# Optimization experiments

Measured on AMD Instinct MI355X. Metric: run time of the kernel, lower is better.

## Reference

```python
import jax, jax.numpy as jnp
import numpy as np

N_NODES = 20000
N_EDGES = 100000
MUL = 128          # channels per irrep
R = 8              # radial (edge scalar) features
H = 64             # radial MLP hidden width
SILU_NORM = 1.6790390826      # e3nn normalize2mom constant for SiLU
INV_SQRT3 = 1.0 / np.sqrt(3.0)   # wigner-3j values for l<=1 paths
PW_0E = np.sqrt(0.5)   # e3nn path weight: out dim 1, fan-in 2 paths
PW_1O = np.sqrt(1.5)   # e3nn path weight: out dim 3, fan-in 2 paths


def setup_inputs() -> dict:
    key = jax.random.key(0)
    ks = jax.random.split(key, 12)
    return dict(
        node_feats=jax.random.normal(ks[0], (N_NODES, 4 * MUL), jnp.float32),
        edge_attrs=jax.random.normal(ks[1], (N_EDGES, 4), jnp.float32),   # SH: 1x0e+1x1o
        edge_feats=jax.random.normal(ks[2], (N_EDGES, R), jnp.float32),
        edge_index=jax.random.randint(ks[3], (2, N_EDGES), 0, N_NODES),
        W_up_s=jax.random.normal(ks[4], (MUL, MUL), jnp.float32),
        W_up_v=jax.random.normal(ks[5], (MUL, MUL), jnp.float32),
        mlp_w0=jax.random.normal(ks[6], (R, H), jnp.float32),
        mlp_w1=jax.random.normal(ks[7], (H, H), jnp.float32),
        mlp_w2=jax.random.normal(ks[8], (H, H), jnp.float32),
        mlp_w3=jax.random.normal(ks[9], (H, 4 * MUL), jnp.float32),
        W_out_s=jax.random.normal(ks[10], (2 * MUL, MUL), jnp.float32),
        W_out_v=jax.random.normal(ks[11], (2 * MUL, MUL), jnp.float32),
    )


def reference(node_feats, edge_attrs, edge_feats, edge_index,
              W_up_s, W_up_v, mlp_w0, mlp_w1, mlp_w2, mlp_w3,
              W_out_s, W_out_v):
    sender = edge_index[0]
    # split node feats into irrep blocks: 128x0e then 128x1o (channel-major [u, m])
    s = node_feats[:, :MUL]                       # [N, 128]
    v = node_feats[:, MUL:].reshape(-1, MUL, 3)   # [N, 128, 3]
    # linear_up: per-irrep e3nn Linear, fan_in-normalized
    s = (s @ W_up_s) / np.sqrt(MUL)
    v = jnp.einsum('nui,uw->nwi', v, W_up_v) / np.sqrt(MUL)
    # radial MLP -> per-edge tensor-product weights (e3nn FullyConnectedNet)
    act = lambda x: jax.nn.silu(x) * SILU_NORM
    h = act(edge_feats @ (mlp_w0 / np.sqrt(R)))
    h = act(h @ (mlp_w1 / np.sqrt(H)))
    h = act(h @ (mlp_w2 / np.sqrt(H)))
    tpw = h @ (mlp_w3 / np.sqrt(H))               # [E, 4*128]
    w00, w01, w10, w11 = jnp.split(tpw, 4, axis=1)  # instruction order of weight_numel
    # gather sender node features per edge
    ss = s[sender]                                # [E, 128]
    vs = v[sender]                                # [E, 128, 3]
    sh0 = edge_attrs[:, :1]                       # [E, 1]  scalar SH
    sh1 = edge_attrs[:, 1:]                       # [E, 3]  l=1 SH
    # uvu CG tensor product paths (l<=1 wigner-3j)
    a0 = PW_0E * w00 * ss * sh0                                   # 0e x 0e -> 0e
    a1 = (PW_1O * INV_SQRT3) * (w01 * ss)[:, :, None] * sh1[:, None, :]   # 0e x 1o -> 1o
    b1 = (PW_1O * INV_SQRT3) * (w10 * sh0)[:, :, None] * vs              # 1o x 0e -> 1o
    b0 = (PW_0E * INV_SQRT3) * w11 * jnp.einsum('eui,ei->eu', vs, sh1)   # 1o x 1o -> 0e
    # irreps_mid sorted+simplified: 256x0e + 256x1o
    mid_s = jnp.concatenate([a0, b0], axis=1)     # [E, 256]
    mid_v = jnp.concatenate([a1, b1], axis=1)     # [E, 256, 3]
    # final per-irrep linear to target 128x0e + 128x1o
    out_s = (mid_s @ W_out_s) / np.sqrt(2 * MUL)
    out_v = jnp.einsum('eui,uw->ewi', mid_v, W_out_v) / np.sqrt(2 * MUL)
    return jnp.concatenate([out_s, out_v.reshape(out_v.shape[0], 3 * MUL)], axis=1)
```

## Files before the change

kernel.cpp:

```cpp
#include <hip/hip_runtime.h>
#include <stdint.h>

#define N_NODES 20000
#define N_EDGES 100000

typedef __bf16 bf16;
typedef bf16  bf16x8 __attribute__((ext_vector_type(8)));
typedef float f32x4  __attribute__((ext_vector_type(4)));

__device__ __forceinline__ f32x4 mfma16(bf16x8 a, bf16x8 b, f32x4 c) {
  return __builtin_amdgcn_mfma_f32_16x16x32_bf16(a, b, c, 0, 0, 0);
}

__device__ __forceinline__ float silu_(float y) {
  return y / (1.0f + __expf(-y));
}

#define OFF_W0T   0u
#define OFF_W1T   4096u
#define OFF_W2T   12288u
#define OFF_W3T   20480u
#define OFF_WOS   86016u
#define OFF_WOV   151552u
#define OFF_WST   217088u
#define OFF_WVT   249856u
#define OFF_SUP   282624u
#define OFF_VUP   5402624u

__global__ __launch_bounds__(256) void k0_prep(
    const float* __restrict__ wus, const float* __restrict__ wuv,
    const float* __restrict__ w0,  const float* __restrict__ w1,
    const float* __restrict__ w2,  const float* __restrict__ w3,
    const float* __restrict__ wos_g, const float* __restrict__ wov_g,
    char* __restrict__ ws) {
  const int idx = blockIdx.x * 256 + threadIdx.x;
  bf16* W0T = (bf16*)(ws + OFF_W0T);
  bf16* W1T = (bf16*)(ws + OFF_W1T);
  bf16* W2T = (bf16*)(ws + OFF_W2T);
  bf16* W3T = (bf16*)(ws + OFF_W3T);
  bf16* WOS = (bf16*)(ws + OFF_WOS);
  bf16* WOV = (bf16*)(ws + OFF_WOV);
  bf16* WST = (bf16*)(ws + OFF_WST);
  bf16* WVT = (bf16*)(ws + OFF_WVT);

  const float cS   = 0.08838834764831845f;
  const float c0   = 0.35355339059327373f;
  const float c12  = 1.6790390826f / 8.0f;
  const float cosA = 0.04419417382415922f;
  const float cosB = 0.025515518153991442f;
  const float cov  = 0.04419417382415922f;

  if (idx < 16384) {
    int w = idx >> 7, u = idx & 127;
    WST[idx] = (bf16)(wus[u * 128 + w] * cS);
    WVT[idx] = (bf16)(wuv[u * 128 + w] * cS);
  }
  if (idx < 2048) {
    int h = idx >> 5, r = idx & 31;
    W0T[idx] = (bf16)((r < 8) ? w0[r * 64 + h] * c0 : 0.0f);
  }
  if (idx < 4096) {
    int h = idx >> 6, k = idx & 63;
    W1T[idx] = (bf16)(w1[k * 64 + h] * c12);
    W2T[idx] = (bf16)(w2[k * 64 + h] * c12);
  }
  {
    int j = idx >> 6, k = idx & 63;
    W3T[idx] = (bf16)(w3[k * 512 + j] * c12);
    int w = idx >> 8, u = idx & 255;
    WOS[idx] = (bf16)(wos_g[u * 128 + w] * ((u < 128) ? cosA : cosB));
    WOV[idx] = (bf16)(wov_g[u * 128 + w] * cov);
  }
}

__global__ __launch_bounds__(256, 4) void k1_nodeup(const float* __restrict__ nf,
                                                    char* __restrict__ ws) {
  __shared__ __align__(16) bf16 tiles[4][32 * 136];
  const int n0 = blockIdx.x * 32;
  const int t = threadIdx.x;

  #pragma unroll
  for (int p = 0; p < 16; p++) {
    int idx = p * 256 + t;
    int r = idx >> 7, c4 = idx & 127;
    const float4 f = *(const float4*)&nf[(size_t)(n0 + r) * 512 + c4 * 4];
    float vals[4] = {f.x, f.y, f.z, f.w};
    #pragma unroll
    for (int e2 = 0; e2 < 4; e2++) {
      int g = c4 * 4 + e2;
      if (g < 128) {
        tiles[0][r * 136 + g] = (bf16)vals[e2];
      } else {
        int gg = g - 128;
        int u = gg / 3, i = gg - 3 * u;
        tiles[1 + i][r * 136 + u] = (bf16)vals[e2];
      }
    }
  }
  __syncthreads();

  const int wv = t >> 6, lane = t & 63;
  const int m = lane & 15, q = lane >> 4;
  const bf16* BT = (const bf16*)(ws + ((wv == 0) ? OFF_WST : OFF_WVT));
  const bf16* At = tiles[wv];

  const f32x4 z = {0.f, 0.f, 0.f, 0.f};
  f32x4 acc[2][8] = {{z, z, z, z, z, z, z, z}, {z, z, z, z, z, z, z, z}};
  #pragma unroll
  for (int kk = 0; kk < 128; kk += 32) {
    bf16x8 af0 = *(const bf16x8*)&At[m * 136 + kk + q * 8];
    bf16x8 af1 = *(const bf16x8*)&At[(16 + m) * 136 + kk + q * 8];
    #pragma unroll
    for (int nt = 0; nt < 8; nt++) {
      bf16x8 bfr = *(const bf16x8*)&BT[(nt * 16 + m) * 128 + kk + q * 8];
      acc[0][nt] = mfma16(af0, bfr, acc[0][nt]);
      acc[1][nt] = mfma16(af1, bfr, acc[1][nt]);
    }
  }

  bf16* sup = (bf16*)(ws + OFF_SUP);
  bf16* vup = (bf16*)(ws + OFF_VUP);
  #pragma unroll
  for (int rt = 0; rt < 2; rt++) {
    #pragma unroll
    for (int nt = 0; nt < 8; nt++) {
      int col = nt * 16 + m;
      #pragma unroll
      for (int r = 0; r < 4; r++) {
        int node = n0 + rt * 16 + q * 4 + r;
        if (wv == 0) sup[node * 128 + col] = (bf16)acc[rt][nt][r];
        else         vup[node * 384 + (wv - 1) * 128 + col] = (bf16)acc[rt][nt][r];
      }
    }
  }
}

#define SM_TPW 0
#define SM_A   33280
#define SM_A0  33280
#define SM_H0  (33280 + 2560)
#define SM_H1  (33280 + 7168)
#define SM_SND 51712
#define SM_ATT 51840
#define TPW_LD 520

__global__ __launch_bounds__(256, 3) void k23_fused(
    const float* __restrict__ efeat, const float* __restrict__ attrs,
    const int* __restrict__ sender, const char* __restrict__ ws,
    float* __restrict__ out) {
  __shared__ __align__(16) char smem[52352];
  bf16* tpwL = (bf16*)(smem + SM_TPW);
  bf16* A    = (bf16*)(smem + SM_A);
  bf16* A0e  = (bf16*)(smem + SM_A0);
  bf16* h0   = (bf16*)(smem + SM_H0);
  bf16* h1   = (bf16*)(smem + SM_H1);
  int*  sLDS = (int*)(smem + SM_SND);
  float* aLDS = (float*)(smem + SM_ATT);

  const int e0 = blockIdx.x * 32;
  const int t = threadIdx.x;
  const int wv = t >> 6, lane = t & 63;
  const int m = lane & 15, q = lane >> 4;
  const f32x4 z = {0.f, 0.f, 0.f, 0.f};

  {
    int r = t >> 3, k = t & 7;
    A0e[r * 40 + k] = (bf16)efeat[(e0 + r) * 8 + k];
    #pragma unroll
    for (int pp = 0; pp < 3; pp++) {
      int pidx = t * 3 + pp;
      int r2 = pidx / 24, k2 = 8 + pidx % 24;
      A0e[r2 * 40 + k2] = (bf16)0.0f;
    }
    if (t < 32) sLDS[t] = sender[e0 + t];
    if (t < 128) aLDS[t] = attrs[e0 * 4 + t];
  }
  __syncthreads();

  const bf16* W0T = (const bf16*)(ws + OFF_W0T);
  const bf16* W1T = (const bf16*)(ws + OFF_W1T);
  const bf16* W2T = (const bf16*)(ws + OFF_W2T);
  const bf16* W3T = (const bf16*)(ws + OFF_W3T);

  const int rt = wv & 1, nh = wv >> 1;

  {
    f32x4 acc[2] = {z, z};
    bf16x8 af = *(const bf16x8*)&A0e[(rt * 16 + m) * 40 + q * 8];
    #pragma unroll
    for (int ntl = 0; ntl < 2; ntl++) {
      int ntg = nh * 2 + ntl;
      bf16x8 bfr = *(const bf16x8*)&W0T[(ntg * 16 + m) * 32 + q * 8];
      acc[ntl] = mfma16(af, bfr, acc[ntl]);
    }
    __syncthreads();
    #pragma unroll
    for (int ntl = 0; ntl < 2; ntl++)
      #pragma unroll
      for (int r = 0; r < 4; r++)
        h0[(rt * 16 + q * 4 + r) * 72 + (nh * 2 + ntl) * 16 + m] = (bf16)silu_(acc[ntl][r]);
  }
  __syncthreads();

  {
    f32x4 acc[2] = {z, z};
    #pragma unroll
    for (int kk = 0; kk < 64; kk += 32) {
      bf16x8 af = *(const bf16x8*)&h0[(rt * 16 + m) * 72 + kk + q * 8];
      #pragma unroll
      for (int ntl = 0; ntl < 2; ntl++) {
        int ntg = nh * 2 + ntl;
        bf16x8 bfr = *(const bf16x8*)&W1T[(ntg * 16 + m) * 64 + kk + q * 8];
        acc[ntl] = mfma16(af, bfr, acc[ntl]);
      }
    }
    __syncthreads();
    #pragma unroll
    for (int ntl = 0; ntl < 2; ntl++)
      #pragma unroll
      for (int r = 0; r < 4; r++)
        h1[(rt * 16 + q * 4 + r) * 72 + (nh * 2 + ntl) * 16 + m] = (bf16)silu_(acc[ntl][r]);
  }
  __syncthreads();

  {
    f32x4 acc[2] = {z, z};
    #pragma unroll
    for (int kk = 0; kk < 64; kk += 32) {
      bf16x8 af = *(const bf16x8*)&h1[(rt * 16 + m) * 72 + kk + q * 8];
      #pragma unroll
      for (int ntl = 0; ntl < 2; ntl++) {
        int ntg = nh * 2 + ntl;
        bf16x8 bfr = *(const bf16x8*)&W2T[(ntg * 16 + m) * 64 + kk + q * 8];
        acc[ntl] = mfma16(af, bfr, acc[ntl]);
      }
    }
    __syncthreads();
    #pragma unroll
    for (int ntl = 0; ntl < 2; ntl++)
      #pragma unroll
      for (int r = 0; r < 4; r++)
        h0[(rt * 16 + q * 4 + r) * 72 + (nh * 2 + ntl) * 16 + m] = (bf16)silu_(acc[ntl][r]);
  }
  __syncthreads();

  {
    bf16x8 af0 = *(const bf16x8*)&h0[(rt * 16 + m) * 72 + 0  + q * 8];
    bf16x8 af1 = *(const bf16x8*)&h0[(rt * 16 + m) * 72 + 32 + q * 8];
    #pragma unroll 4
    for (int i = 0; i < 16; i++) {
      int ntg = nh * 16 + i;
      f32x4 acc = z;
      bf16x8 b0 = *(const bf16x8*)&W3T[(ntg * 16 + m) * 64 + q * 8];
      bf16x8 b1 = *(const bf16x8*)&W3T[(ntg * 16 + m) * 64 + 32 + q * 8];
      acc = mfma16(af0, b0, acc);
      acc = mfma16(af1, b1, acc);
      int col = ntg * 16 + m;
      #pragma unroll
      for (int r = 0; r < 4; r++)
        tpwL[(rt * 16 + q * 4 + r) * TPW_LD + col] = (bf16)acc[r];
    }
  }
  __syncthreads();

  const bf16* sup = (const bf16*)(ws + OFF_SUP);
  const bf16* vup = (const bf16*)(ws + OFF_VUP);
  const bf16* WB = (const bf16*)(ws + ((wv == 0) ? OFF_WOS : OFF_WOV));

  const int srow = t >> 1;
  const int kh = (t & 1) * 32;
  const bool isS = (srow < 32);
  const int ii = isS ? 0 : ((srow - 32) >> 5);
  const int eL = isS ? srow : ((srow - 32) & 31);
  const int se = sLDS[eL];
  const float s0  = aLDS[eL * 4 + 0];
  const float s1x = aLDS[eL * 4 + 1];
  const float s1y = aLDS[eL * 4 + 2];
  const float s1z = aLDS[eL * 4 + 3];
  const float s1i = (ii == 0) ? s1x : ((ii == 1) ? s1y : s1z);
  const bf16* tpr = tpwL + eL * TPW_LD;
  const bf16* supR = sup + se * 128;
  const bf16* vupR = vup + se * 384;

  f32x4 acc0[8] = {z, z, z, z, z, z, z, z};
  f32x4 acc1[8] = {z, z, z, z, z, z, z, z};

  for (int kc = 0; kc < 4; kc++) {
    if (kc) __syncthreads();
    if (kc < 2) {
      const int ub = kc * 64 + kh;
      if (isS) {
        #pragma unroll
        for (int j0 = 0; j0 < 32; j0 += 8) {
          bf16x8 tv = *(const bf16x8*)&tpr[ub + j0];
          bf16x8 sv = *(const bf16x8*)&supR[ub + j0];
          bf16x8 o;
          #pragma unroll
          for (int e = 0; e < 8; e++)
            o[e] = (bf16)((float)tv[e] * (float)sv[e] * s0);
          *(bf16x8*)&A[srow * 72 + kh + j0] = o;
        }
      } else {
        #pragma unroll
        for (int j0 = 0; j0 < 32; j0 += 8) {
          bf16x8 tv = *(const bf16x8*)&tpr[128 + ub + j0];
          bf16x8 sv = *(const bf16x8*)&supR[ub + j0];
          bf16x8 o;
          #pragma unroll
          for (int e = 0; e < 8; e++)
            o[e] = (bf16)((float)tv[e] * (float)sv[e] * s1i);
          *(bf16x8*)&A[srow * 72 + kh + j0] = o;
        }
      }
    } else {
      const int ub = (kc - 2) * 64 + kh;
      if (isS) {
        #pragma unroll
        for (int j0 = 0; j0 < 32; j0 += 8) {
          bf16x8 tv = *(const bf16x8*)&tpr[384 + ub + j0];
          bf16x8 vx = *(const bf16x8*)&vupR[ub + j0];
          bf16x8 vy = *(const bf16x8*)&vupR[128 + ub + j0];
          bf16x8 vz = *(const bf16x8*)&vupR[256 + ub + j0];
          bf16x8 o;
          #pragma unroll
          for (int e = 0; e < 8; e++) {
            float dv = (float)vx[e] * s1x + (float)vy[e] * s1y + (float)vz[e] * s1z;
            o[e] = (bf16)((float)tv[e] * dv);
          }
          *(bf16x8*)&A[srow * 72 + kh + j0] = o;
        }
      } else {
        #pragma unroll
        for (int j0 = 0; j0 < 32; j0 += 8) {
          bf16x8 tv = *(const bf16x8*)&tpr[256 + ub + j0];
          bf16x8 vv = *(const bf16x8*)&vupR[ii * 128 + ub + j0];
          bf16x8 o;
          #pragma unroll
          for (int e = 0; e < 8; e++)
            o[e] = (bf16)((float)tv[e] * s0 * (float)vv[e]);
          *(bf16x8*)&A[srow * 72 + kh + j0] = o;
        }
      }
    }
    __syncthreads();

    const int kb = kc * 64;
    #pragma unroll
    for (int kk = 0; kk < 64; kk += 32) {
      bf16x8 af0 = *(const bf16x8*)&A[(wv * 32 + m) * 72 + kk + q * 8];
      bf16x8 af1 = *(const bf16x8*)&A[(wv * 32 + 16 + m) * 72 + kk + q * 8];
      #pragma unroll
      for (int nt = 0; nt < 8; nt++) {
        bf16x8 bfr = *(const bf16x8*)&WB[(nt * 16 + m) * 256 + kb + kk + q * 8];
        acc0[nt] = mfma16(af0, bfr, acc0[nt]);
        acc1[nt] = mfma16(af1, bfr, acc1[nt]);
      }
    }
  }

  #pragma unroll
  for (int b = 0; b < 2; b++) {
    const f32x4* accp = b ? acc1 : acc0;
    int rb = wv * 32 + b * 16 + q * 4;
    #pragma unroll
    for (int nt = 0; nt < 8; nt++) {
      int col = nt * 16 + m;
      #pragma unroll
      for (int r = 0; r < 4; r++) {
        int row = rb + r;
        float v = accp[nt][r];
        if (wv == 0) {
          out[(size_t)(e0 + row) * 512 + col] = v;
        } else {
          int i2 = (row - 32) >> 5, eL2 = (row - 32) & 31;
          out[(size_t)(e0 + eL2) * 512 + 128 + 3 * col + i2] = v;
        }
      }
    }
  }
}

extern "C" void kernel_launch(void* const* d_in, const int* in_sizes, int n_in,
                              void* d_out, int out_size, void* d_ws, size_t ws_size,
                              hipStream_t stream) {
  const float* node_feats = (const float*)d_in[0];
  const float* edge_attrs = (const float*)d_in[1];
  const float* edge_feats = (const float*)d_in[2];
  const int*   edge_index = (const int*)d_in[3];
  const float* W_up_s = (const float*)d_in[4];
  const float* W_up_v = (const float*)d_in[5];
  const float* w0 = (const float*)d_in[6];
  const float* w1 = (const float*)d_in[7];
  const float* w2 = (const float*)d_in[8];
  const float* w3 = (const float*)d_in[9];
  const float* Wos = (const float*)d_in[10];
  const float* Wov = (const float*)d_in[11];
  float* out = (float*)d_out;
  char* ws = (char*)d_ws;

  k0_prep<<<dim3(128), dim3(256), 0, stream>>>(W_up_s, W_up_v, w0, w1, w2, w3,
                                               Wos, Wov, ws);
  k1_nodeup<<<dim3(625), dim3(256), 0, stream>>>(node_feats, ws);
  k23_fused<<<dim3(3125), dim3(256), 0, stream>>>(edge_feats, edge_attrs,
                                                  edge_index, ws, out);
}
```

Baseline: 458.4 us.

## Async-gather sender features into swizzled LDS and build MFMA fragments in registers

Sender rows of sup/vup are prefetched with global_load_lds into XOR-swizzled LDS at kernel start, so the gather overlaps with the radial MLP. The A-operand staging tile in LDS is removed; each wave builds its tensor-product MFMA fragments directly in registers from the LDS copies of tpw, sup and vup. The tpw output is computed in two halves to shrink LDS to about 49KB, and edge features are loaded straight into registers, dropping several barriers. The cost is more per-wave ALU work and register pressure, plus the need for the swizzle and the async loads to be correctly ordered before first use.

```diff
diff --git a/kernel.cpp b/kernel.cpp
--- a/kernel.cpp
+++ b/kernel.cpp
@@ -135,27 +135,76 @@
   }
 }
 
-#define SM_TPW 0
-#define SM_A   33280
-#define SM_A0  33280
-#define SM_H0  (33280 + 2560)
-#define SM_H1  (33280 + 7168)
-#define SM_SND 51712
-#define SM_ATT 51840
-#define TPW_LD 520
+#define L_TPW   0
+#define L_H0    0
+#define L_H1    4608
+#define L_SUP   16896
+#define L_VUP   25088
+#define L_TOT   49664
+#define TPW_LD  264
+
+#define GLOAD_LDS16(gsrc, ldst) __builtin_amdgcn_global_load_lds( \
+    (const __attribute__((address_space(1))) void*)(gsrc),        \
+    (__attribute__((address_space(3))) void*)(ldst), 16, 0, 0)
+
+__device__ __forceinline__ bf16x8 ldsw8(const bf16* row, int elem, int sw) {
+  int c = elem >> 3;
+  int cs = (c & ~7) | ((c ^ sw) & 7);
+  return *(const bf16x8*)&row[cs * 8];
+}
+
+__device__ __forceinline__ bf16x8 build_frag(
+    int wv, int ii, int kc, int off ,
+    const bf16* tpr, const bf16* supR, const bf16* vupR, int sw,
+    float4 at, float s1i) {
+  bf16x8 af;
+  if (kc < 2) {
+    const int K = kc * 64 + off;
+    bf16x8 sv = ldsw8(supR, K, sw);
+    if (wv == 0) {
+      bf16x8 tv = *(const bf16x8*)&tpr[K];
+      #pragma unroll
+      for (int j = 0; j < 8; j++)
+        af[j] = (bf16)((float)tv[j] * (float)sv[j] * at.x);
+    } else {
+      bf16x8 tv = *(const bf16x8*)&tpr[128 + K];
+      #pragma unroll
+      for (int j = 0; j < 8; j++)
+        af[j] = (bf16)((float)tv[j] * (float)sv[j] * s1i);
+    }
+  } else {
+    const int Kl = (kc - 2) * 64 + off;
+    if (wv == 0) {
+      bf16x8 tv = *(const bf16x8*)&tpr[128 + Kl];
+      bf16x8 vx = ldsw8(vupR, Kl, sw);
+      bf16x8 vy = ldsw8(vupR, 128 + Kl, sw);
+      bf16x8 vz = ldsw8(vupR, 256 + Kl, sw);
+      #pragma unroll
+      for (int j = 0; j < 8; j++) {
+        float dv = (float)vx[j] * at.y + (float)vy[j] * at.z + (float)vz[j] * at.w;
+        af[j] = (bf16)((float)tv[j] * dv);
+      }
+    } else {
+      bf16x8 tv = *(const bf16x8*)&tpr[Kl];
+      bf16x8 vv = ldsw8(vupR, ii * 128 + Kl, sw);
+      #pragma unroll
+      for (int j = 0; j < 8; j++)
+        af[j] = (bf16)((float)tv[j] * at.x * (float)vv[j]);
+    }
+  }
+  return af;
+}
 
 __global__ __launch_bounds__(256, 3) void k23_fused(
     const float* __restrict__ efeat, const float* __restrict__ attrs,
     const int* __restrict__ sender, const char* __restrict__ ws,
     float* __restrict__ out) {
-  __shared__ __align__(16) char smem[52352];
-  bf16* tpwL = (bf16*)(smem + SM_TPW);
-  bf16* A    = (bf16*)(smem + SM_A);
-  bf16* A0e  = (bf16*)(smem + SM_A0);
-  bf16* h0   = (bf16*)(smem + SM_H0);
-  bf16* h1   = (bf16*)(smem + SM_H1);
-  int*  sLDS = (int*)(smem + SM_SND);
-  float* aLDS = (float*)(smem + SM_ATT);
+  __shared__ __align__(16) char smem[L_TOT];
+  bf16* tpwH = (bf16*)(smem + L_TPW);
+  bf16* h0   = (bf16*)(smem + L_H0);
+  bf16* h1   = (bf16*)(smem + L_H1);
+  bf16* supL = (bf16*)(smem + L_SUP);
+  bf16* vupL = (bf16*)(smem + L_VUP);
 
   const int e0 = blockIdx.x * 32;
   const int t = threadIdx.x;
@@ -164,18 +213,27 @@
   const f32x4 z = {0.f, 0.f, 0.f, 0.f};
 
   {
-    int r = t >> 3, k = t & 7;
-    A0e[r * 40 + k] = (bf16)efeat[(e0 + r) * 8 + k];
-    #pragma unroll
-    for (int pp = 0; pp < 3; pp++) {
-      int pidx = t * 3 + pp;
-      int r2 = pidx / 24, k2 = 8 + pidx % 24;
-      A0e[r2 * 40 + k2] = (bf16)0.0f;
-    }
-    if (t < 32) sLDS[t] = sender[e0 + t];
-    if (t < 128) aLDS[t] = attrs[e0 * 4 + t];
-  }
-  __syncthreads();
+    #pragma unroll
+    for (int jj = 0; jj < 2; jj++) {
+      int j = wv * 2 + jj;
+      int f = j * 64 + lane;
+      int e = f >> 4, c = f & 15;
+      int se = sender[e0 + e];
+      int cs = c ^ (e & 7);
+      GLOAD_LDS16(ws + OFF_SUP + (size_t)se * 256 + cs * 16,
+                  (char*)supL + j * 1024);
+    }
+    #pragma unroll
+    for (int jj = 0; jj < 6; jj++) {
+      int j = wv * 6 + jj;
+      int f = j * 64 + lane;
+      int e = f / 48, c = f - e * 48;
+      int se = sender[e0 + e];
+      int cs = (c & ~7) | ((c ^ e) & 7);
+      GLOAD_LDS16(ws + OFF_VUP + (size_t)se * 768 + cs * 16,
+                  (char*)vupL + j * 1024);
+    }
+  }
 
   const bf16* W0T = (const bf16*)(ws + OFF_W0T);
   const bf16* W1T = (const bf16*)(ws + OFF_W1T);
@@ -185,15 +243,22 @@
   const int rt = wv & 1, nh = wv >> 1;
 
   {
+    bf16x8 af;
+    #pragma unroll
+    for (int j = 0; j < 8; j++) af[j] = (bf16)0.0f;
+    if (q == 0) {
+      const float4* ef4 = (const float4*)efeat;
+      float4 u0 = ef4[(size_t)(e0 + rt * 16 + m) * 2 + 0];
+      float4 u1 = ef4[(size_t)(e0 + rt * 16 + m) * 2 + 1];
+      af[0] = (bf16)u0.x; af[1] = (bf16)u0.y; af[2] = (bf16)u0.z; af[3] = (bf16)u0.w;
+      af[4] = (bf16)u1.x; af[5] = (bf16)u1.y; af[6] = (bf16)u1.z; af[7] = (bf16)u1.w;
+    }
     f32x4 acc[2] = {z, z};
-    bf16x8 af = *(const bf16x8*)&A0e[(rt * 16 + m) * 40 + q * 8];
     #pragma unroll
     for (int ntl = 0; ntl < 2; ntl++) {
-      int ntg = nh * 2 + ntl;
-      bf16x8 bfr = *(const bf16x8*)&W0T[(ntg * 16 + m) * 32 + q * 8];
+      bf16x8 bfr = *(const bf16x8*)&W0T[((nh * 2 + ntl) * 16 + m) * 32 + q * 8];
       acc[ntl] = mfma16(af, bfr, acc[ntl]);
     }
-    __syncthreads();
     #pragma unroll
     for (int ntl = 0; ntl < 2; ntl++)
       #pragma unroll
@@ -209,12 +274,10 @@
       bf16x8 af = *(const bf16x8*)&h0[(rt * 16 + m) * 72 + kk + q * 8];
       #pragma unroll
       for (int ntl = 0; ntl < 2; ntl++) {
-        int ntg = nh * 2 + ntl;
-        bf16x8 bfr = *(const bf16x8*)&W1T[(ntg * 16 + m) * 64 + kk + q * 8];
+        bf16x8 bfr = *(const bf16x8*)&W1T[((nh * 2 + ntl) * 16 + m) * 64 + kk + q * 8];
         acc[ntl] = mfma16(af, bfr, acc[ntl]);
       }
     }
-    __syncthreads();
     #pragma unroll
     for (int ntl = 0; ntl < 2; ntl++)
       #pragma unroll
@@ -230,8 +293,7 @@
       bf16x8 af = *(const bf16x8*)&h1[(rt * 16 + m) * 72 + kk + q * 8];
       #pragma unroll
       for (int ntl = 0; ntl < 2; ntl++) {
-        int ntg = nh * 2 + ntl;
-        bf16x8 bfr = *(const bf16x8*)&W2T[(ntg * 16 + m) * 64 + kk + q * 8];
+        bf16x8 bfr = *(const bf16x8*)&W2T[((nh * 2 + ntl) * 16 + m) * 64 + kk + q * 8];
         acc[ntl] = mfma16(af, bfr, acc[ntl]);
       }
     }
@@ -244,116 +306,64 @@
   }
   __syncthreads();
 
-  {
-    bf16x8 af0 = *(const bf16x8*)&h0[(rt * 16 + m) * 72 + 0  + q * 8];
-    bf16x8 af1 = *(const bf16x8*)&h0[(rt * 16 + m) * 72 + 32 + q * 8];
-    #pragma unroll 4
-    for (int i = 0; i < 16; i++) {
-      int ntg = nh * 16 + i;
-      f32x4 acc = z;
-      bf16x8 b0 = *(const bf16x8*)&W3T[(ntg * 16 + m) * 64 + q * 8];
-      bf16x8 b1 = *(const bf16x8*)&W3T[(ntg * 16 + m) * 64 + 32 + q * 8];
-      acc = mfma16(af0, b0, acc);
-      acc = mfma16(af1, b1, acc);
-      int col = ntg * 16 + m;
-      #pragma unroll
-      for (int r = 0; r < 4; r++)
-        tpwL[(rt * 16 + q * 4 + r) * TPW_LD + col] = (bf16)acc[r];
-    }
-  }
+  bf16x8 hf0 = *(const bf16x8*)&h0[(rt * 16 + m) * 72 + 0  + q * 8];
+  bf16x8 hf1 = *(const bf16x8*)&h0[(rt * 16 + m) * 72 + 32 + q * 8];
   __syncthreads();
 
-  const bf16* sup = (const bf16*)(ws + OFF_SUP);
-  const bf16* vup = (const bf16*)(ws + OFF_VUP);
+  const int eA = m, eB = 16 + m;
+  const int sw = m & 7;
+  const float4* at4 = (const float4*)attrs;
+  const float4 atA = at4[e0 + eA];
+  const float4 atB = at4[e0 + eB];
+  const int ii = wv - 1;
+  const float s1A = (ii == 0) ? atA.y : ((ii == 1) ? atA.z : atA.w);
+  const float s1B = (ii == 0) ? atB.y : ((ii == 1) ? atB.z : atB.w);
+  const bf16* tprA = tpwH + eA * TPW_LD;
+  const bf16* tprB = tpwH + eB * TPW_LD;
+  const bf16* supA = supL + eA * 128;
+  const bf16* supB = supL + eB * 128;
+  const bf16* vupA = vupL + eA * 384;
+  const bf16* vupB = vupL + eB * 384;
   const bf16* WB = (const bf16*)(ws + ((wv == 0) ? OFF_WOS : OFF_WOV));
-
-  const int srow = t >> 1;
-  const int kh = (t & 1) * 32;
-  const bool isS = (srow < 32);
-  const int ii = isS ? 0 : ((srow - 32) >> 5);
-  const int eL = isS ? srow : ((srow - 32) & 31);
-  const int se = sLDS[eL];
-  const float s0  = aLDS[eL * 4 + 0];
-  const float s1x = aLDS[eL * 4 + 1];
-  const float s1y = aLDS[eL * 4 + 2];
-  const float s1z = aLDS[eL * 4 + 3];
-  const float s1i = (ii == 0) ? s1x : ((ii == 1) ? s1y : s1z);
-  const bf16* tpr = tpwL + eL * TPW_LD;
-  const bf16* supR = sup + se * 128;
-  const bf16* vupR = vup + se * 384;
 
   f32x4 acc0[8] = {z, z, z, z, z, z, z, z};
   f32x4 acc1[8] = {z, z, z, z, z, z, z, z};
 
-  for (int kc = 0; kc < 4; kc++) {
-    if (kc) __syncthreads();
-    if (kc < 2) {
-      const int ub = kc * 64 + kh;
-      if (isS) {
+  #pragma unroll
+  for (int half = 0; half < 2; half++) {
+    if (half) __syncthreads();
+
+    {
+      #pragma unroll 2
+      for (int i = 0; i < 8; i++) {
+        int ntg = (wv >> 1) * 8 + i;
+        f32x4 acc = z;
+        const bf16* wb = &W3T[(size_t)((half * 16 + ntg) * 16 + m) * 64 + q * 8];
+        bf16x8 b0 = *(const bf16x8*)&wb[0];
+        bf16x8 b1 = *(const bf16x8*)&wb[32];
+        acc = mfma16(hf0, b0, acc);
+        acc = mfma16(hf1, b1, acc);
         #pragma unroll
-        for (int j0 = 0; j0 < 32; j0 += 8) {
-          bf16x8 tv = *(const bf16x8*)&tpr[ub + j0];
-          bf16x8 sv = *(const bf16x8*)&supR[ub + j0];
-          bf16x8 o;
-          #pragma unroll
-          for (int e = 0; e < 8; e++)
-            o[e] = (bf16)((float)tv[e] * (float)sv[e] * s0);
-          *(bf16x8*)&A[srow * 72 + kh + j0] = o;
+        for (int r = 0; r < 4; r++)
+          tpwH[(rt * 16 + q * 4 + r) * TPW_LD + ntg * 16 + m] = (bf16)acc[r];
+      }
+    }
+    __syncthreads();
+
+    #pragma unroll
+    for (int kci = 0; kci < 2; kci++) {
+      const int kc = half * 2 + kci;
+      const int kb = kc * 64;
+      #pragma unroll
+      for (int kk = 0; kk < 64; kk += 32) {
+        bf16x8 af0 = build_frag(wv, ii, kc, kk + q * 8, tprA, supA, vupA, sw, atA, s1A);
+        bf16x8 af1 = build_frag(wv, ii, kc, kk + q * 8, tprB, supB, vupB, sw, atB, s1B);
+        #pragma unroll
+        for (int nt = 0; nt < 8; nt++) {
+          bf16x8 bfr = *(const bf16x8*)&WB[(nt * 16 + m) * 256 + kb + kk + q * 8];
+          acc0[nt] = mfma16(af0, bfr, acc0[nt]);
+          acc1[nt] = mfma16(af1, bfr, acc1[nt]);
         }
-      } else {
-        #pragma unroll
-        for (int j0 = 0; j0 < 32; j0 += 8) {
-          bf16x8 tv = *(const bf16x8*)&tpr[128 + ub + j0];
-          bf16x8 sv = *(const bf16x8*)&supR[ub + j0];
-          bf16x8 o;
-          #pragma unroll
-          for (int e = 0; e < 8; e++)
-            o[e] = (bf16)((float)tv[e] * (float)sv[e] * s1i);
-          *(bf16x8*)&A[srow * 72 + kh + j0] = o;
-        }
-      }
-    } else {
-      const int ub = (kc - 2) * 64 + kh;
-      if (isS) {
-        #pragma unroll
-        for (int j0 = 0; j0 < 32; j0 += 8) {
-          bf16x8 tv = *(const bf16x8*)&tpr[384 + ub + j0];
-          bf16x8 vx = *(const bf16x8*)&vupR[ub + j0];
-          bf16x8 vy = *(const bf16x8*)&vupR[128 + ub + j0];
-          bf16x8 vz = *(const bf16x8*)&vupR[256 + ub + j0];
-          bf16x8 o;
-          #pragma unroll
-          for (int e = 0; e < 8; e++) {
-            float dv = (float)vx[e] * s1x + (float)vy[e] * s1y + (float)vz[e] * s1z;
-            o[e] = (bf16)((float)tv[e] * dv);
-          }
-          *(bf16x8*)&A[srow * 72 + kh + j0] = o;
-        }
-      } else {
-        #pragma unroll
-        for (int j0 = 0; j0 < 32; j0 += 8) {
-          bf16x8 tv = *(const bf16x8*)&tpr[256 + ub + j0];
-          bf16x8 vv = *(const bf16x8*)&vupR[ii * 128 + ub + j0];
-          bf16x8 o;
-          #pragma unroll
-          for (int e = 0; e < 8; e++)
-            o[e] = (bf16)((float)tv[e] * s0 * (float)vv[e]);
-          *(bf16x8*)&A[srow * 72 + kh + j0] = o;
-        }
-      }
-    }
-    __syncthreads();
-
-    const int kb = kc * 64;
-    #pragma unroll
-    for (int kk = 0; kk < 64; kk += 32) {
-      bf16x8 af0 = *(const bf16x8*)&A[(wv * 32 + m) * 72 + kk + q * 8];
-      bf16x8 af1 = *(const bf16x8*)&A[(wv * 32 + 16 + m) * 72 + kk + q * 8];
-      #pragma unroll
-      for (int nt = 0; nt < 8; nt++) {
-        bf16x8 bfr = *(const bf16x8*)&WB[(nt * 16 + m) * 256 + kb + kk + q * 8];
-        acc0[nt] = mfma16(af0, bfr, acc0[nt]);
-        acc1[nt] = mfma16(af1, bfr, acc1[nt]);
       }
     }
   }
```

Result: no change. 464.5 us (+1.3%).
